# Optimization experiments

Hardware: AMD Instinct MI355X
Metric: run time of the kernel (lower is better)

## Reference

```python
import jax, jax.numpy as jnp
import numpy as np
from jax import lax

SCALES = [0.5, 0.25, 0.125, 0.0625]
D_MODEL = 256
IN_CH = 1


def setup_inputs() -> dict:
    key = jax.random.key(0)
    ks = jax.random.split(key, 16)
    x = jax.random.normal(ks[0], (2, D_MODEL, 256, 256), dtype=jnp.float32)
    m = jax.random.uniform(ks[1], (2, IN_CH, 256, 256), dtype=jnp.float32)
    s = 0.05
    Wq = jax.random.normal(ks[2], (D_MODEL, D_MODEL, 1, 1), jnp.float32) * s
    bq = jax.random.normal(ks[3], (D_MODEL,), jnp.float32) * s
    Wk = jax.random.normal(ks[4], (D_MODEL, D_MODEL, 1, 1), jnp.float32) * s
    bk = jax.random.normal(ks[5], (D_MODEL,), jnp.float32) * s
    Wv = jax.random.normal(ks[6], (D_MODEL, D_MODEL, 1, 1), jnp.float32) * s
    bv = jax.random.normal(ks[7], (D_MODEL,), jnp.float32) * s
    Wmq = jax.random.normal(ks[8], (D_MODEL, IN_CH, 1, 1), jnp.float32) * s
    bmq = jax.random.normal(ks[9], (D_MODEL,), jnp.float32) * s
    Wmk = jax.random.normal(ks[10], (D_MODEL, IN_CH, 1, 1), jnp.float32) * s
    bmk = jax.random.normal(ks[11], (D_MODEL,), jnp.float32) * s
    Wo = jax.random.normal(ks[12], (D_MODEL, D_MODEL, 3, 3), jnp.float32) * s
    bo = jax.random.normal(ks[13], (D_MODEL,), jnp.float32) * s
    return {"x": x, "m": m, "Wq": Wq, "bq": bq, "Wk": Wk, "bk": bk,
            "Wv": Wv, "bv": bv, "Wmq": Wmq, "bmq": bmq, "Wmk": Wmk, "bmk": bmk,
            "Wo": Wo, "bo": bo, "b": 1, "c": 256}


def _conv1x1(z, W, bias):
    # W: (O, I, 1, 1)
    return jnp.einsum('bihw,oi->bohw', z, W[:, :, 0, 0]) + bias[None, :, None, None]


def _forward(x, m, Wq, bq, Wk, bk, Wv, bv, Wmq, bmq, Wmk, bmk, Wo, bo, b, c):
    bt, _, h, w = x.shape  # h, w are multiples of 64 -> pad is zero
    t = bt // b
    n_scales = len(SCALES)
    d_k = c // n_scales

    q = _conv1x1(x, Wq, bq)
    k = _conv1x1(x, Wk, bk)
    v = _conv1x1(x, Wv, bv)
    mq = _conv1x1(m, Wmq, bmq)
    mk = _conv1x1(m, Wmk, bmk)

    outs = []
    for i, scale in enumerate(SCALES):
        height, width = int(h * scale), int(w * scale)
        out_h, out_w = h // height, w // width
        sl = slice(i * d_k, (i + 1) * d_k)

        def patch(z):
            # (b, t, d_k, out_h, height, out_w, width) -> (b, t*out_h*out_w, d_k*height*width)
            z = z[:, sl].reshape(b, t, d_k, out_h, height, out_w, width)
            z = z.transpose(0, 1, 3, 5, 2, 4, 6)
            return z.reshape(b, t * out_h * out_w, d_k * height * width)

        Q, K, V = patch(q), patch(k), patch(v)
        MQ, MK = patch(mq), patch(mk)
        inv_sqrt_d = 1.0 / jnp.sqrt(jnp.asarray(Q.shape[-1], jnp.float32))
        scores = jnp.einsum('bnd,bmd->bnm', Q, K) * inv_sqrt_d
        mask_scores = jnp.einsum('bnd,bmd->bnm', MQ, MK) * inv_sqrt_d
        p_attn = jax.nn.softmax(scores * mask_scores, axis=-1)
        y = jnp.einsum('bnm,bmd->bnd', p_attn, V)
        # back to (bt, d_k, h, w)
        y = y.reshape(b, t, out_h, out_w, d_k, height, width)
        y = y.transpose(0, 1, 4, 2, 5, 3, 6).reshape(bt, d_k, h, w)
        outs.append(y)

    out = jnp.concatenate(outs, axis=1)
    z = lax.conv_general_dilated(out, Wo, window_strides=(1, 1),
                                 padding=((1, 1), (1, 1)),
                                 dimension_numbers=('NCHW', 'OIHW', 'NCHW'))
    z = z + bo[None, :, None, None]
    return jnp.where(z > 0, z, 0.2 * z)  # LeakyReLU(0.2)


def reference(x, m, Wq, bq, Wk, bk, Wv, bv, Wmq, bmq, Wmk, bmk, Wo, bo, b, c):
    return _forward(x, m, Wq, bq, Wk, bk, Wv, bv, Wmq, bmq, Wmk, bmk, Wo, bo, b, c)
```

## Files before the change

kernel.cpp:

```cpp
#include <hip/hip_runtime.h>
#include <stdint.h>


typedef __attribute__((ext_vector_type(8))) short short8;
typedef __attribute__((ext_vector_type(4))) float floatx4;
typedef __attribute__((ext_vector_type(4))) unsigned int uintx4;

#define DEV static __device__ __forceinline__

DEV unsigned short f2bf(float f) {
  unsigned u = __builtin_bit_cast(unsigned, f);
  unsigned r = u + 0x7FFFu + ((u >> 16) & 1u);
  return (unsigned short)(r >> 16);
}

DEV void patch_row(int n, int sc, int lw, int& pt, int& sp0) {
  pt = n >> (2 + 2 * sc);
  int rem = n & ((4 << (2 * sc)) - 1);
  int oh = rem >> (1 + sc), ow = rem & ((2 << sc) - 1);
  sp0 = (oh << (lw + 8)) + (ow << lw);
}

__global__ void k_prep(const float* __restrict__ Wq, const float* __restrict__ Wk,
                       const float* __restrict__ Wv, const float* __restrict__ bq,
                       const float* __restrict__ bk, const float* __restrict__ bv,
                       const float* __restrict__ Wmq, const float* __restrict__ bmq,
                       const float* __restrict__ Wmk, const float* __restrict__ bmk,
                       const float* __restrict__ Wo, const float* __restrict__ bo,
                       unsigned short* __restrict__ wqkv, float* __restrict__ bias,
                       float* __restrict__ msc, unsigned short* __restrict__ wobf,
                       float* __restrict__ scoresG, unsigned int* __restrict__ pbuf) {
  int bid = blockIdx.x;
  int t = threadIdx.x;
  if (bid < 768) {
    const float* src = bid < 256 ? (Wq + bid * 256) : (bid < 512 ? (Wk + (bid - 256) * 256)
                                                                 : (Wv + (bid - 512) * 256));
    wqkv[bid * 256 + t] = f2bf(src[t]);
    if (t == 0) bias[bid] = bid < 256 ? bq[bid] : (bid < 512 ? bk[bid - 256] : bv[bid - 512]);
    return;
  }
  if (bid == 768) {
    int sc = t >> 6, lane = t & 63;
    int ch = sc * 64 + lane;
    float a0 = Wmq[ch] * Wmk[ch];
    float a1 = Wmq[ch] * bmk[ch];
    float a2 = bmq[ch] * Wmk[ch];
    float a3 = bmq[ch] * bmk[ch];
    for (int off = 32; off; off >>= 1) {
      a0 += __shfl_xor(a0, off); a1 += __shfl_xor(a1, off);
      a2 += __shfl_xor(a2, off); a3 += __shfl_xor(a3, off);
    }
    if (lane == 0) {
      msc[sc * 4 + 0] = a0; msc[sc * 4 + 1] = a1;
      msc[sc * 4 + 2] = a2; msc[sc * 4 + 3] = a3;
    }
    return;
  }
  int blk = bid - 769;
  if (blk < 2304) {
    int didx = blk >> 8, o = blk & 255, c = t;
    wobf[didx * 65536 + o * 256 + c] = f2bf(Wo[o * 2304 + c * 9 + didx]);
  } else {
    int i = (blk - 2304) * 256 + t;
    if (i < 559232) scoresG[i] = 0.f;
    if (i < 140032) pbuf[i] = 0u;
  }
}

__global__ __launch_bounds__(256) void k_xt(const float* __restrict__ x,
                                            unsigned short* __restrict__ xt) {
  __shared__ __align__(16) unsigned short tile[64][72];
  int p0 = blockIdx.x * 64, c0 = blockIdx.y * 64, t = blockIdx.z;
  int tid = threadIdx.x;
  {
    int cc = tid >> 2, pq = (tid & 3) * 16;
    const float* src = x + ((t * 256 + c0 + cc) * 65536 + p0 + pq);
    __align__(16) unsigned short tmp[16];
#pragma unroll
    for (int e = 0; e < 16; e += 4) {
      floatx4 v = *(const floatx4*)(src + e);
      tmp[e + 0] = f2bf(v[0]); tmp[e + 1] = f2bf(v[1]);
      tmp[e + 2] = f2bf(v[2]); tmp[e + 3] = f2bf(v[3]);
    }
    *(uintx4*)&tile[cc][pq] = *(const uintx4*)&tmp[0];
    *(uintx4*)&tile[cc][pq + 8] = *(const uintx4*)&tmp[8];
  }
  __syncthreads();
  {
    int pp = tid >> 2, cg = (tid & 3) * 16;
    __align__(16) unsigned short outv[16];
#pragma unroll
    for (int e = 0; e < 16; ++e) outv[e] = tile[cg + e][pp];
    unsigned short* dst = xt + ((t * 65536 + p0 + pp) * 256 + c0 + cg);
    *(uintx4*)dst = *(const uintx4*)&outv[0];
    *(uintx4*)(dst + 8) = *(const uintx4*)&outv[8];
  }
}

__global__ __launch_bounds__(256) void k_yt(const unsigned short* __restrict__ ynat,
                                            unsigned short* __restrict__ yt) {
  __shared__ __align__(16) unsigned short tile[64][72];
  int p0 = blockIdx.x * 64, c0 = blockIdx.y * 64, t = blockIdx.z;
  int tid = threadIdx.x;
  {
    int cc = tid >> 2, pq = (tid & 3) * 16;
    const unsigned short* src = ynat + ((t * 256 + c0 + cc) * 65536 + p0 + pq);
    *(uintx4*)&tile[cc][pq] = *(const uintx4*)src;
    *(uintx4*)&tile[cc][pq + 8] = *(const uintx4*)(src + 8);
  }
  __syncthreads();
  {
    int pp = tid >> 2, cg = (tid & 3) * 16;
    __align__(16) unsigned short outv[16];
#pragma unroll
    for (int e = 0; e < 16; ++e) outv[e] = tile[cg + e][pp];
    unsigned short* dst = yt + ((t * 65536 + p0 + pp) * 256 + c0 + cg);
    *(uintx4*)dst = *(const uintx4*)&outv[0];
    *(uintx4*)(dst + 8) = *(const uintx4*)&outv[8];
  }
}

__global__ __launch_bounds__(256, 2) void k_qkv(const unsigned short* __restrict__ xt,
                                                const unsigned short* __restrict__ wqkv,
                                                const float* __restrict__ bias,
                                                unsigned short* __restrict__ qkv) {
  extern __shared__ __align__(16) char smem[];
  auto As = (unsigned short (*)[64])(smem);
  auto Bs = (unsigned short (*)[64])(smem + 16384);
  auto Cs = (unsigned short (*)[280])(smem);
  int flat = blockIdx.x;
  int lg = (flat & 7) * 384 + (flat >> 3);
  int n_t = lg / 6, m_t = lg - n_t * 6;
  int n0 = n_t << 8, m0 = m_t << 7;
  int tid = threadIdx.x;
  int w = tid >> 6, l = tid & 63;
  int wr = w >> 1, wc = w & 1;
  int l15 = l & 15, lhi = l >> 4;
  int sr = tid >> 1, sbase = (tid & 1) * 4, r7 = sr & 7;
  int b7 = tid & 7;
  const unsigned short* gA = wqkv + (m0 + sr) * 256 + sbase * 8;
  const unsigned short* gB = xt + (n0 + tid) * 256;
  floatx4 zf = {0.f, 0.f, 0.f, 0.f};
  floatx4 acc[4][8];
#pragma unroll
  for (int i = 0; i < 4; ++i)
#pragma unroll
    for (int j = 0; j < 8; ++j) acc[i][j] = zf;
  uintx4 ra[4], rb[8];
#define QLOAD(K0) { const uintx4* pa = (const uintx4*)(gA + (K0)); \
                    ra[0] = pa[0]; ra[1] = pa[1]; ra[2] = pa[2]; ra[3] = pa[3]; \
                    const uintx4* pb = (const uintx4*)(gB + (K0)); \
                    rb[0] = pb[0]; rb[1] = pb[1]; rb[2] = pb[2]; rb[3] = pb[3]; \
                    rb[4] = pb[4]; rb[5] = pb[5]; rb[6] = pb[6]; rb[7] = pb[7]; }
  QLOAD(0);
#pragma unroll
  for (int ch = 0; ch < 4; ++ch) {
    __syncthreads();
#pragma unroll
    for (int j = 0; j < 4; ++j)
      *(uintx4*)&As[sr][((sbase + j) ^ r7) * 8] = ra[j];
#pragma unroll
    for (int j = 0; j < 8; ++j)
      *(uintx4*)&Bs[tid][(j ^ b7) * 8] = rb[j];
    __syncthreads();
    if (ch < 3) QLOAD((ch + 1) * 64);
#pragma unroll
    for (int kk = 0; kk < 2; ++kk) {
      short8 af[4];
#pragma unroll
      for (int f = 0; f < 4; ++f) {
        int arow = wr * 64 + f * 16 + l15;
        af[f] = *(const short8*)&As[arow][(((kk << 2) + lhi) ^ (arow & 7)) * 8];
      }
#pragma unroll
      for (int fn = 0; fn < 8; ++fn) {
        int brow = wc * 128 + fn * 16 + l15;
        short8 b = *(const short8*)&Bs[brow][(((kk << 2) + lhi) ^ (brow & 7)) * 8];
#pragma unroll
        for (int fm = 0; fm < 4; ++fm)
          acc[fm][fn] = __builtin_amdgcn_mfma_f32_16x16x32_bf16(af[fm], b, acc[fm][fn], 0, 0, 0);
      }
    }
  }
#undef QLOAD
#pragma unroll
  for (int h = 0; h < 2; ++h) {
    __syncthreads();
    if (wr == h) {
#pragma unroll
      for (int fm = 0; fm < 4; ++fm) {
#pragma unroll
        for (int rr = 0; rr < 4; ++rr) {
          int rl = fm * 16 + lhi * 4 + rr;
          float bv = bias[m0 + h * 64 + rl];
#pragma unroll
          for (int fn = 0; fn < 8; ++fn)
            Cs[rl][wc * 128 + fn * 16 + l15] = f2bf(acc[fm][fn][rr] + bv);
        }
      }
    }
    __syncthreads();
    {
      int p8 = (tid & 31) * 8;
      int pcol = n0 + p8;
      int t = pcol >> 16, p = pcol & 65535;
#pragma unroll
      for (int pass = 0; pass < 8; ++pass) {
        int rl = (tid >> 5) + pass * 8;
        uintx4 v = *(const uintx4*)&Cs[rl][p8];
        *(uintx4*)&qkv[((t * 768 + m0 + h * 64 + rl) << 16) + p] = v;
      }
    }
  }
}

__global__ __launch_bounds__(256) void k_mask(const float* __restrict__ m,
                                              float* __restrict__ G,
                                              float* __restrict__ rbuf) {
  int bid = blockIdx.x;
  int tid = threadIdx.x;
  if (bid >= 328) {
    int row = (bid - 328) * 4 + (tid >> 6);
    int lane = tid & 63;
    if (row < 680) {
      int sc, n;
      if (row < 8)        { sc = 0; n = row; }
      else if (row < 40)  { sc = 1; n = row - 8; }
      else if (row < 168) { sc = 2; n = row - 40; }
      else                { sc = 3; n = row - 168; }
      int lw = 7 - sc, W = 1 << lw;
      int pt, sp0;
      patch_row(n, sc, lw, pt, sp0);
      int base = pt * 65536 + sp0;
      int S = 1 << (14 - 2 * sc);
      float acc = 0.f;
      for (int s = lane; s < S; s += 64) {
        int hh = s >> lw, ww = s & (W - 1);
        acc += m[base + (hh << 8) + ww];
      }
      for (int off = 32; off; off >>= 1) acc += __shfl_xor(acc, off);
      if (lane == 0) rbuf[row] = acc;
    }
    return;
  }
  __shared__ __align__(16) float Ns[32][68];
// ... 9 lines not shown
  bool isA = tid < 128;
  int u = tid & 127;
  int srow = u >> 2, sslot0 = (u & 3) * 4;
  int grow = (isA ? n0 : m0) + srow;
  bool valid = grow < N;
  int pt = 0, sp0 = 0;
  if (valid) patch_row(grow, sc, lw, pt, sp0);
  int gbase = pt * 65536 + sp0;
  int trc = tid >> 4, tcc = tid & 15;
  float a00 = 0.f, a01 = 0.f, a10 = 0.f, a11 = 0.f;
  floatx4 zf = {0.f, 0.f, 0.f, 0.f};
  for (int c = 0; c < nchunks; ++c) {
    int k0 = kbase + c * 64;
    floatx4 v[4];
#pragma unroll
    for (int j = 0; j < 4; ++j) {
      v[j] = zf;
      if (valid) {
        int s = k0 + (sslot0 + j) * 4;
        int hh = s >> lw, ww = s & (W - 1);
        v[j] = *(const floatx4*)(m + gbase + (hh << 8) + ww);
      }
    }
    __syncthreads();
    float* dstrow = isA ? &Ns[srow][0] : &Ms[srow][0];
#pragma unroll
    for (int j = 0; j < 4; ++j) *(floatx4*)&dstrow[(sslot0 + j) * 4] = v[j];
    __syncthreads();
#pragma unroll 4
    for (int k = 0; k < 64; k += 4) {
      floatx4 na = *(const floatx4*)&Ns[2 * trc][k];
      floatx4 nb = *(const floatx4*)&Ns[2 * trc + 1][k];
      floatx4 ma = *(const floatx4*)&Ms[2 * tcc][k];
      floatx4 mb = *(const floatx4*)&Ms[2 * tcc + 1][k];
#pragma unroll
      for (int e = 0; e < 4; ++e) {
        a00 += na[e] * ma[e]; a01 += na[e] * mb[e];
        a10 += nb[e] * ma[e]; a11 += nb[e] * mb[e];
      }
    }
  }
  int rn = n0 + 2 * trc, rm = m0 + 2 * tcc;
  float res[2][2] = {{a00, a01}, {a10, a11}};
#pragma unroll
  for (int i = 0; i < 2; ++i)
#pragma unroll
    for (int j = 0; j < 2; ++j) {
      if (rn + i < N && rm + j < N) {
        float* dst = &G[soff + (rn + i) * N + rm + j];
        if (sc < 3) atomicAdd(dst, res[i][j]); else *dst = res[i][j];
      }
    }
}

__global__ __launch_bounds__(256) void k_scores_all(const unsigned short* __restrict__ qkv,
                                                    float* __restrict__ scores) {
  __shared__ __align__(16) char sbuf[32768];
  int bid = blockIdx.x;
  int tid = threadIdx.x;
  int w = tid >> 6, l = tid & 63;
  int wr = w >> 1, wc = w & 1, l15 = l & 15, lhi = l >> 4;
  uintx4 zu = {0u, 0u, 0u, 0u};
  floatx4 zf = {0.f, 0.f, 0.f, 0.f};
  if (bid < 160) {
    auto As = (unsigned short (*)[64])(sbuf);
    auto Bs = (unsigned short (*)[64])(sbuf + 16384);
    int lg = (bid & 7) * 20 + (bid >> 3);
    int sc, tn, tm, z, soff;
    if (lg < 32) { sc = 2; tn = 0; tm = 0; z = lg; soff = 1088; }
    else { int r = lg - 32; int tl = r >> 3; sc = 3; tn = tl >> 2; tm = tl & 3; z = r & 7; soff = 17472; }
    int N = 8 << (2 * sc);
    int lw = 7 - sc, W = 1 << lw, lS = 14 - 2 * sc;
    int n0 = tn * 128, m0 = tm * 128;
    int kbase = z * 2048;
    int sr = tid >> 1, sbase = (tid & 1) * 4, r7 = sr & 7;
    int ptA, spA, ptB, spB;
    patch_row(n0 + sr, sc, lw, ptA, spA);
    patch_row(m0 + sr, sc, lw, ptB, spB);
    int baseA = (ptA * 768 + sc * 64) * 65536 + spA;
    int baseB = (ptB * 768 + 256 + sc * 64) * 65536 + spB;
    floatx4 acc[4][4];
#pragma unroll
    for (int i = 0; i < 4; ++i)
#pragma unroll
      for (int j = 0; j < 4; ++j) acc[i][j] = zf;
    uintx4 ra[4], rb[4];
#define GLOAD(K0) { \
  _Pragma("unroll") for (int j = 0; j < 4; ++j) { \
    int k = kbase + (K0) + (sbase + j) * 8; \
    int cl = k >> lS; int s = k & ((1 << lS) - 1); \
    int hh = s >> lw, ww = s & (W - 1); \
    int off = cl * 65536 + (hh << 8) + ww; \
    ra[j] = *(const uintx4*)(qkv + baseA + off); \
    rb[j] = *(const uintx4*)(qkv + baseB + off); } }
    GLOAD(0);
    for (int st = 0; st < 32; ++st) {
      __syncthreads();
#pragma unroll
      for (int j = 0; j < 4; ++j) {
        *(uintx4*)&As[sr][((sbase + j) ^ r7) * 8] = ra[j];
        *(uintx4*)&Bs[sr][((sbase + j) ^ r7) * 8] = rb[j];
      }
      __syncthreads();
      if (st < 31) GLOAD((st + 1) * 64);
#pragma unroll
      for (int kk = 0; kk < 2; ++kk) {
        short8 af[4], bfr[4];
#pragma unroll
        for (int f = 0; f < 4; ++f) {
          int arow = wr * 64 + f * 16 + l15;
          af[f] = *(const short8*)&As[arow][(((kk << 2) + lhi) ^ (arow & 7)) * 8];
          int brow = wc * 64 + f * 16 + l15;
          bfr[f] = *(const short8*)&Bs[brow][(((kk << 2) + lhi) ^ (brow & 7)) * 8];
        }
#pragma unroll
        for (int fm = 0; fm < 4; ++fm)
#pragma unroll
          for (int fn = 0; fn < 4; ++fn)
            acc[fm][fn] = __builtin_amdgcn_mfma_f32_16x16x32_bf16(af[fm], bfr[fn], acc[fm][fn], 0, 0, 0);
      }
    }
#undef GLOAD
#pragma unroll
    for (int fm = 0; fm < 4; ++fm) {
      int nrow = n0 + wr * 64 + fm * 16 + lhi * 4;
#pragma unroll
      for (int rr = 0; rr < 4; ++rr) {
#pragma unroll
        for (int fn = 0; fn < 4; ++fn) {
          int mcol = m0 + wc * 64 + fn * 16 + l15;
          atomicAdd(&scores[soff + (nrow + rr) * N + mcol], acc[fm][fn][rr]);
        }
      }
    }
    return;
  }
  {
    auto As = (unsigned short (*)[136])(sbuf);
    auto Bs = (unsigned short (*)[136])(sbuf + 8704);
    int b2 = bid - 160;
    int sc, z, soff;
    if (b2 < 256) { sc = 0; z = b2;       soff = 0; }
    else          { sc = 1; z = b2 - 256; soff = 64; }
    int lw = 7 - sc, W = 1 << lw, lS = 14 - 2 * sc, N = 8 << (2 * sc);
    int kbase = z * 4096;
    floatx4 acc = zf;
    bool isA = tid < 128;
    int u = tid & 127;
    int srow = u >> 2, sslot0 = (u & 3) * 4;
    int grow = srow;
    int cb = (isA ? 0 : 256) + sc * 64;
    int pt = 0, sp0 = 0;
    bool valid = grow < N;
    if (valid) patch_row(grow, sc, lw, pt, sp0);
    int rowbase = (pt * 768 + cb) * 65536 + sp0;
    uintx4 r[4];
#define SLOAD(KS) { int kb2 = kbase + (KS) * 128; \
  _Pragma("unroll") for (int j = 0; j < 4; ++j) { \
    uintx4 v = zu; \
    if (valid) { int k = kb2 + (sslot0 + j) * 8; \
      int cl = k >> lS; int s = k & ((1 << lS) - 1); \
      int hh = s >> lw, ww = s & (W - 1); \
      v = *(const uintx4*)(qkv + rowbase + cl * 65536 + (hh << 8) + ww); } \
    r[j] = v; } }
    SLOAD(0);
    for (int ks = 0; ks < 32; ++ks) {
      __syncthreads();
      {
        unsigned short* dstrow = isA ? &As[srow][0] : &Bs[srow][0];
#pragma unroll
        for (int j = 0; j < 4; ++j) *(uintx4*)&dstrow[(sslot0 + j) * 8] = r[j];
      }
      __syncthreads();
// ... 39 lines not shown
    float v = -1e30f;
    int mcol = lane + j * 64;
    if (j * 64 < N && mcol < N) {
      float sq = scores[soff + n * N + mcol];
      float g = G[soff + n * N + mcol];
      float rm = rbuf[roff + mcol];
      v = sq * (alpha * g + beta * rn + gamma * rm + delta * Sf) * invD;
    }
    vals[j] = v;
    mx = fmaxf(mx, v);
  }
  for (int off = 32; off; off >>= 1) mx = fmaxf(mx, __shfl_xor(mx, off));
  float sum = 0.f;
#pragma unroll
  for (int j = 0; j < 8; ++j) {
    int mcol = lane + j * 64;
    float e = 0.f;
    if (j * 64 < N && mcol < N) e = __expf(vals[j] - mx);
    vals[j] = e;
    sum += e;
  }
  for (int off = 32; off; off >>= 1) sum += __shfl_xor(sum, off);
  float inv = 1.f / sum;
#pragma unroll
  for (int j = 0; j < 8; ++j) {
    int mcol = lane + j * 64;
    if (j * 64 < N && mcol < N) pbuf[poff + n * Kpad + mcol] = f2bf(vals[j] * inv);
  }
}

__global__ __launch_bounds__(256) void k_pv(const unsigned short* __restrict__ qkv,
                                            const unsigned short* __restrict__ pbuf,
                                            unsigned short* __restrict__ ynat) {
  int bid = blockIdx.x;
  int sc, bx, by;
  if (bid < 4096)      { sc = 0; bx = bid; by = 0; }
  else if (bid < 6144) { sc = 1; bx = bid - 4096; by = 0; }
  else if (bid < 8192) { int r = bid - 6144; sc = 2; bx = r >> 1; by = r & 1; }
  else                 { int r = bid - 8192; sc = 3; bx = r >> 3; by = r & 7; }
  int WR    = (sc == 0) ? 1 : (sc == 1) ? 2 : 4;
  int logWC = (sc == 0) ? 2 : (sc == 1) ? 1 : 0;
  int poff  = (sc == 0) ? 0 : (sc == 1) ? 512 : (sc == 2) ? 1536 : 17920;
  int lw = 7 - sc, W = 1 << lw;
  int lS = 14 - 2 * sc;
  int N = 8 << (2 * sc);
  int Kpad = (sc < 2) ? 32 : N;
  int WC = 1 << logWC;
  int d0 = bx * (WC * 64);
  int nb = by * (WR * 16);
  __shared__ __align__(16) unsigned short As[2][64][40];
  __shared__ __align__(16) unsigned short Bt[2][256][32];
  int tid = threadIdx.x;
  int w = tid >> 6, l = tid & 63;
  int wr = w >> logWC, wc = w & (WC - 1);
  int l15 = l & 15, lhi = l >> 4;
  floatx4 zf = {0.f, 0.f, 0.f, 0.f};
  floatx4 acc[4];
#pragma unroll
  for (int i = 0; i < 4; ++i) acc[i] = zf;
  int bmp = tid & 15;
  int dg = tid >> 4;
  bool act0 = (WC > 1) || (dg < 8);
  bool has1 = (WC == 4);
  bool doA = tid < WR * 64;
  int arow = tid >> 2, akg = (tid & 3) * 8;
  int ksteps = Kpad >> 5;
  uintx4 zu = {0u, 0u, 0u, 0u};
// ... 45 lines not shown
    }
    __syncthreads();
    if (ks + 1 < ksteps) PLOADS(ks + 1);
    short8 a = *(const short8*)&As[b][wr * 16 + l15][lhi * 8];
#pragma unroll
    for (int fn = 0; fn < 4; ++fn) {
      int row = wc * 64 + fn * 16 + l15;
      int slot = lhi ^ ((row >> 1) & 3) ^ ((row >> 3) & 3);
      short8 bb = *(const short8*)&Bt[b][row][slot * 8];
      acc[fn] = __builtin_amdgcn_mfma_f32_16x16x32_bf16(a, bb, acc[fn], 0, 0, 0);
    }
  }
#undef PLOADS
  int nrow = nb + wr * 16 + lhi * 4;
#pragma unroll
  for (int rr = 0; rr < 4; ++rr) {
    int n = nrow + rr;
    if (n < N) {
      int pt, sp0;
      patch_row(n, sc, lw, pt, sp0);
#pragma unroll
      for (int fn = 0; fn < 4; ++fn) {
        int d = d0 + wc * 64 + fn * 16 + l15;
        int cl = d >> lS;
        int s = d & ((1 << lS) - 1);
        int hh = s >> lw, ww = s & (W - 1);
        int c = sc * 64 + cl;
        ynat[(pt * 256 + c) * 65536 + sp0 + (hh << 8) + ww] = f2bf(acc[fn][rr]);
      }
    }
  }
}

__global__ __launch_bounds__(256, 3) void k_conv(const unsigned short* __restrict__ yt,
                                                 const unsigned short* __restrict__ wo,
                                                 const float* __restrict__ bo,
                                                 float* __restrict__ out) {
  __shared__ __align__(16) unsigned short As[64][128];
  __shared__ __align__(16) unsigned short Bs[130][64];
  int flat = blockIdx.x;
  int lg = ((flat & 7) << 8) + (flat >> 3);
  int n_t = lg >> 2, m_t = lg & 3;
  int n0 = n_t << 8, m0 = m_t << 6;
  int tt = n0 >> 16, yy = (n0 >> 8) & 255;
  int tid = threadIdx.x;
  int w = tid >> 6, l = tid & 63;
  int l15 = l & 15, lhi = l >> 4;
  bool doA = tid < 192;
  int a_dx = tid >> 6, a_o = tid & 63;
  bool doBh = tid >= 254;
  floatx4 zf = {0.f, 0.f, 0.f, 0.f};
  floatx4 acc[4][4];
#pragma unroll
  for (int i = 0; i < 4; ++i)
#pragma unroll
    for (int j = 0; j < 4; ++j) acc[i][j] = zf;
  uintx4 zu = {0u, 0u, 0u, 0u};
  uintx4 rb[4], ra[4], rh[4];
  const unsigned short* ybase = yt + (tt << 24);
#define CLOAD(ST) { \
    int dy = (ST) >> 3, cc = ((ST) & 7) << 5; \
    int yq = yy + dy - 1; \
    bool yv = (unsigned)yq < 256u; \
    { int xq = tid - 1; \
      if (yv && (unsigned)xq < 256u) { \
        const uintx4* p = (const uintx4*)(ybase + ((yq << 8) + xq) * 256 + cc); \
        rb[0] = p[0]; rb[1] = p[1]; rb[2] = p[2]; rb[3] = p[3]; \
      } else { rb[0] = zu; rb[1] = zu; rb[2] = zu; rb[3] = zu; } } \
    if (doA) { \
      const uintx4* p = (const uintx4*)(wo + (dy * 3 + a_dx) * 65536 + (m0 + a_o) * 256 + cc); \
      ra[0] = p[0]; ra[1] = p[1]; ra[2] = p[2]; ra[3] = p[3]; \
    } else if (doBh) { \
      int xq = tid + 1;   \
      if (yv && xq < 256) { \
        const uintx4* p = (const uintx4*)(ybase + ((yq << 8) + xq) * 256 + cc); \
        rh[0] = p[0]; rh[1] = p[1]; rh[2] = p[2]; rh[3] = p[3]; \
      } else { rh[0] = zu; rh[1] = zu; rh[2] = zu; rh[3] = zu; } } }
  CLOAD(0);
  for (int st = 0; st < 24; ++st) {
    __syncthreads();
    {
      int brow = tid >> 1, bhf = (tid & 1) * 4, br7 = brow & 7;
#pragma unroll
      for (int j = 0; j < 4; ++j)
        *(uintx4*)&Bs[brow][((bhf + j) ^ br7) * 8] = rb[j];
      if (doA) {
        int o7 = a_o & 7;
#pragma unroll
        for (int j = 0; j < 4; ++j)
          *(uintx4*)&As[a_o][((a_dx * 4 + j) ^ o7) * 8] = ra[j];
      } else if (doBh) {
        int xh = tid + 2;
        int brow2 = xh >> 1, bhf2 = (xh & 1) * 4, br72 = brow2 & 7;
#pragma unroll
        for (int j = 0; j < 4; ++j)
          *(uintx4*)&Bs[brow2][((bhf2 + j) ^ br72) * 8] = rh[j];
      }
    }
    __syncthreads();
    if (st < 23) CLOAD(st + 1);
#pragma unroll
    for (int dx = 0; dx < 3; ++dx) {
      short8 af[4];
#pragma unroll
      for (int f = 0; f < 4; ++f) {
        int ol = f * 16 + l15;
        af[f] = *(const short8*)&As[ol][((dx * 4 + lhi) ^ (ol & 7)) * 8];
      }
#pragma unroll
      for (int fn = 0; fn < 4; ++fn) {
        int xh = w * 64 + fn * 16 + l15 + dx;
        short8 b = *(const short8*)&Bs[xh >> 1][((((xh & 1) * 4 + lhi)) ^ ((xh >> 1) & 7)) * 8];
#pragma unroll
        for (int fm = 0; fm < 4; ++fm)
          acc[fm][fn] = __builtin_amdgcn_mfma_f32_16x16x32_bf16(af[fm], b, acc[fm][fn], 0, 0, 0);
      }
    }
  }
#undef CLOAD
#pragma unroll
  for (int fm = 0; fm < 4; ++fm) {
    int o = m0 + fm * 16 + lhi * 4;
#pragma unroll
    for (int rr = 0; rr < 4; ++rr) {
      float bias = bo[o + rr];
#pragma unroll
      for (int fn = 0; fn < 4; ++fn) {
        int xcol = w * 64 + fn * 16 + l15;
        float z = acc[fm][fn][rr] + bias;
        out[((tt * 256 + o + rr) << 16) + (yy << 8) + xcol] = z > 0.f ? z : 0.2f * z;
      }
    }
  }
}

extern "C" void kernel_launch(void* const* d_in, const int* in_sizes, int n_in,
                              void* d_out, int out_size, void* d_ws, size_t ws_size,
                              hipStream_t stream) {
  const float* x   = (const float*)d_in[0];
  const float* m   = (const float*)d_in[1];
  const float* Wq  = (const float*)d_in[2];
  const float* bq  = (const float*)d_in[3];
  const float* Wk  = (const float*)d_in[4];
  const float* bk  = (const float*)d_in[5];
  const float* Wv  = (const float*)d_in[6];
  const float* bv  = (const float*)d_in[7];
  const float* Wmq = (const float*)d_in[8];
  const float* bmq = (const float*)d_in[9];
  const float* Wmk = (const float*)d_in[10];
  const float* bmk = (const float*)d_in[11];
  const float* Wo  = (const float*)d_in[12];
  const float* bo  = (const float*)d_in[13];

  char* ws = (char*)d_ws;
  unsigned short* qkv   = (unsigned short*)(ws);
  unsigned short* xtb   = (unsigned short*)(ws + 201326592);
  unsigned short* wqkv  = (unsigned short*)(ws + 268435456);
  unsigned short* wobf  = (unsigned short*)(ws + 268828672);
  float* bias           = (float*)(ws + 270008320);
  float* msc            = (float*)(ws + 270011392);
  float* scores         = (float*)(ws + 270011456);
  float* G              = (float*)(ws + 271129920);
  float* rbuf           = (float*)(ws + 272248384);
  unsigned short* pbuf  = (unsigned short*)(ws + 272251104);
  float* out            = (float*)d_out;
  unsigned short* ynat  = (unsigned short*)d_out;

  k_prep<<<dim3(5258), dim3(256), 0, stream>>>(Wq, Wk, Wv, bq, bk, bv, Wmq, bmq, Wmk, bmk,
                                               Wo, bo, wqkv, bias, msc, wobf, scores,
                                               (unsigned int*)pbuf);
  k_xt<<<dim3(1024, 4, 2), dim3(256), 0, stream>>>(x, xtb);
  k_qkv<<<dim3(3072), dim3(256), 49152, stream>>>(xtb, wqkv, bias, qkv);
  k_mask<<<dim3(498), dim3(256), 0, stream>>>(m, G, rbuf);
  k_scores_all<<<dim3(480), dim3(256), 0, stream>>>(qkv, scores);
  k_softmax<<<dim3(680), dim3(64), 0, stream>>>(scores, G, rbuf, msc, pbuf);
  k_pv<<<dim3(10240), dim3(256), 0, stream>>>(qkv, pbuf, ynat);
  k_yt<<<dim3(1024, 4, 2), dim3(256), 0, stream>>>(ynat, xtb);
  k_conv<<<dim3(2048), dim3(256), 0, stream>>>(xtb, wobf, bo, out);
}
```

Before: 576.4 us.

## Retile 3x3 conv as full-row GEMM, split scores K more, remap PV blocks

The output 3x3 conv is rebuilt as a 512-thread block computing all 256 output channels for a full image row. It uses a tap-major weight layout (o, tap, c) and a double-buffered LDS pipeline over 36 K-steps, replacing the previous 64-channel tiles with halo handling. The split-K factor for the small-scale score GEMMs is doubled to give more blocks, at the cost of more atomic adds. PV block indices for the larger scales are permuted for better cache locality, and some kernels are reordered in the file. The larger conv tile raises register and LDS use and cuts occupancy to one block per CU, with fewer blocks overall.

```diff
diff --git a/kernel.cpp b/kernel.cpp
--- a/kernel.cpp
+++ b/kernel.cpp
@@ -21,14 +21,14 @@
   sp0 = (oh << (lw + 8)) + (ow << lw);
 }
 
-__global__ void k_prep(const float* __restrict__ Wq, const float* __restrict__ Wk,
+__global__ __launch_bounds__(256) void k_prep(const float* __restrict__ Wq, const float* __restrict__ Wk,
                        const float* __restrict__ Wv, const float* __restrict__ bq,
                        const float* __restrict__ bk, const float* __restrict__ bv,
                        const float* __restrict__ Wmq, const float* __restrict__ bmq,
                        const float* __restrict__ Wmk, const float* __restrict__ bmk,
-                       const float* __restrict__ Wo, const float* __restrict__ bo,
+                       const float* __restrict__ Wo,
                        unsigned short* __restrict__ wqkv, float* __restrict__ bias,
-                       float* __restrict__ msc, unsigned short* __restrict__ wobf,
+                       float* __restrict__ msc, unsigned short* __restrict__ wo3,
                        float* __restrict__ scoresG, unsigned int* __restrict__ pbuf) {
   int bid = blockIdx.x;
   int t = threadIdx.x;
@@ -59,158 +59,11 @@
   int blk = bid - 769;
   if (blk < 2304) {
     int didx = blk >> 8, o = blk & 255, c = t;
-    wobf[didx * 65536 + o * 256 + c] = f2bf(Wo[o * 2304 + c * 9 + didx]);
+    wo3[o * 2304 + didx * 256 + c] = f2bf(Wo[o * 2304 + c * 9 + didx]);
   } else {
     int i = (blk - 2304) * 256 + t;
     if (i < 559232) scoresG[i] = 0.f;
     if (i < 140032) pbuf[i] = 0u;
-  }
-}
-
-__global__ __launch_bounds__(256) void k_xt(const float* __restrict__ x,
-                                            unsigned short* __restrict__ xt) {
-  __shared__ __align__(16) unsigned short tile[64][72];
-  int p0 = blockIdx.x * 64, c0 = blockIdx.y * 64, t = blockIdx.z;
-  int tid = threadIdx.x;
-  {
-    int cc = tid >> 2, pq = (tid & 3) * 16;
-    const float* src = x + ((t * 256 + c0 + cc) * 65536 + p0 + pq);
-    __align__(16) unsigned short tmp[16];
-#pragma unroll
-    for (int e = 0; e < 16; e += 4) {
-      floatx4 v = *(const floatx4*)(src + e);
-      tmp[e + 0] = f2bf(v[0]); tmp[e + 1] = f2bf(v[1]);
-      tmp[e + 2] = f2bf(v[2]); tmp[e + 3] = f2bf(v[3]);
-    }
-    *(uintx4*)&tile[cc][pq] = *(const uintx4*)&tmp[0];
-    *(uintx4*)&tile[cc][pq + 8] = *(const uintx4*)&tmp[8];
-  }
-  __syncthreads();
-  {
-    int pp = tid >> 2, cg = (tid & 3) * 16;
-    __align__(16) unsigned short outv[16];
-#pragma unroll
-    for (int e = 0; e < 16; ++e) outv[e] = tile[cg + e][pp];
-    unsigned short* dst = xt + ((t * 65536 + p0 + pp) * 256 + c0 + cg);
-    *(uintx4*)dst = *(const uintx4*)&outv[0];
-    *(uintx4*)(dst + 8) = *(const uintx4*)&outv[8];
-  }
-}
-
-__global__ __launch_bounds__(256) void k_yt(const unsigned short* __restrict__ ynat,
-                                            unsigned short* __restrict__ yt) {
-  __shared__ __align__(16) unsigned short tile[64][72];
-  int p0 = blockIdx.x * 64, c0 = blockIdx.y * 64, t = blockIdx.z;
-  int tid = threadIdx.x;
-  {
-    int cc = tid >> 2, pq = (tid & 3) * 16;
-    const unsigned short* src = ynat + ((t * 256 + c0 + cc) * 65536 + p0 + pq);
-    *(uintx4*)&tile[cc][pq] = *(const uintx4*)src;
-    *(uintx4*)&tile[cc][pq + 8] = *(const uintx4*)(src + 8);
-  }
-  __syncthreads();
-  {
-    int pp = tid >> 2, cg = (tid & 3) * 16;
-    __align__(16) unsigned short outv[16];
-#pragma unroll
-    for (int e = 0; e < 16; ++e) outv[e] = tile[cg + e][pp];
-    unsigned short* dst = yt + ((t * 65536 + p0 + pp) * 256 + c0 + cg);
-    *(uintx4*)dst = *(const uintx4*)&outv[0];
-    *(uintx4*)(dst + 8) = *(const uintx4*)&outv[8];
-  }
-}
-
-__global__ __launch_bounds__(256, 2) void k_qkv(const unsigned short* __restrict__ xt,
-                                                const unsigned short* __restrict__ wqkv,
-                                                const float* __restrict__ bias,
-                                                unsigned short* __restrict__ qkv) {
-  extern __shared__ __align__(16) char smem[];
-  auto As = (unsigned short (*)[64])(smem);
-  auto Bs = (unsigned short (*)[64])(smem + 16384);
-  auto Cs = (unsigned short (*)[280])(smem);
-  int flat = blockIdx.x;
-  int lg = (flat & 7) * 384 + (flat >> 3);
-  int n_t = lg / 6, m_t = lg - n_t * 6;
-  int n0 = n_t << 8, m0 = m_t << 7;
-  int tid = threadIdx.x;
-  int w = tid >> 6, l = tid & 63;
-  int wr = w >> 1, wc = w & 1;
-  int l15 = l & 15, lhi = l >> 4;
-  int sr = tid >> 1, sbase = (tid & 1) * 4, r7 = sr & 7;
-  int b7 = tid & 7;
-  const unsigned short* gA = wqkv + (m0 + sr) * 256 + sbase * 8;
-  const unsigned short* gB = xt + (n0 + tid) * 256;
-  floatx4 zf = {0.f, 0.f, 0.f, 0.f};
-  floatx4 acc[4][8];
-#pragma unroll
-  for (int i = 0; i < 4; ++i)
-#pragma unroll
-    for (int j = 0; j < 8; ++j) acc[i][j] = zf;
-  uintx4 ra[4], rb[8];
-#define QLOAD(K0) { const uintx4* pa = (const uintx4*)(gA + (K0)); \
-                    ra[0] = pa[0]; ra[1] = pa[1]; ra[2] = pa[2]; ra[3] = pa[3]; \
-                    const uintx4* pb = (const uintx4*)(gB + (K0)); \
-                    rb[0] = pb[0]; rb[1] = pb[1]; rb[2] = pb[2]; rb[3] = pb[3]; \
-                    rb[4] = pb[4]; rb[5] = pb[5]; rb[6] = pb[6]; rb[7] = pb[7]; }
-  QLOAD(0);
-#pragma unroll
-  for (int ch = 0; ch < 4; ++ch) {
-    __syncthreads();
-#pragma unroll
-    for (int j = 0; j < 4; ++j)
-      *(uintx4*)&As[sr][((sbase + j) ^ r7) * 8] = ra[j];
-#pragma unroll
-    for (int j = 0; j < 8; ++j)
-      *(uintx4*)&Bs[tid][(j ^ b7) * 8] = rb[j];
-    __syncthreads();
-    if (ch < 3) QLOAD((ch + 1) * 64);
-#pragma unroll
-    for (int kk = 0; kk < 2; ++kk) {
-      short8 af[4];
-#pragma unroll
-      for (int f = 0; f < 4; ++f) {
-        int arow = wr * 64 + f * 16 + l15;
-        af[f] = *(const short8*)&As[arow][(((kk << 2) + lhi) ^ (arow & 7)) * 8];
-      }
-#pragma unroll
-      for (int fn = 0; fn < 8; ++fn) {
-        int brow = wc * 128 + fn * 16 + l15;
-        short8 b = *(const short8*)&Bs[brow][(((kk << 2) + lhi) ^ (brow & 7)) * 8];
-#pragma unroll
-        for (int fm = 0; fm < 4; ++fm)
-          acc[fm][fn] = __builtin_amdgcn_mfma_f32_16x16x32_bf16(af[fm], b, acc[fm][fn], 0, 0, 0);
-      }
-    }
-  }
-#undef QLOAD
-#pragma unroll
-  for (int h = 0; h < 2; ++h) {
-    __syncthreads();
-    if (wr == h) {
-#pragma unroll
-      for (int fm = 0; fm < 4; ++fm) {
-#pragma unroll
-        for (int rr = 0; rr < 4; ++rr) {
-          int rl = fm * 16 + lhi * 4 + rr;
-          float bv = bias[m0 + h * 64 + rl];
-#pragma unroll
-          for (int fn = 0; fn < 8; ++fn)
-            Cs[rl][wc * 128 + fn * 16 + l15] = f2bf(acc[fm][fn][rr] + bv);
-        }
-      }
-    }
-    __syncthreads();
-    {
-      int p8 = (tid & 31) * 8;
-      int pcol = n0 + p8;
-      int t = pcol >> 16, p = pcol & 65535;
-#pragma unroll
-      for (int pass = 0; pass < 8; ++pass) {
-        int rl = (tid >> 5) + pass * 8;
-        uintx4 v = *(const uintx4*)&Cs[rl][p8];
-        *(uintx4*)&qkv[((t * 768 + m0 + h * 64 + rl) << 16) + p] = v;
-      }
-    }
   }
 }
 
@@ -286,11 +139,11 @@
       floatx4 na = *(const floatx4*)&Ns[2 * trc][k];
       floatx4 nb = *(const floatx4*)&Ns[2 * trc + 1][k];
       floatx4 ma = *(const floatx4*)&Ms[2 * tcc][k];
-      floatx4 mb = *(const floatx4*)&Ms[2 * tcc + 1][k];
+      floatx4 mb2 = *(const floatx4*)&Ms[2 * tcc + 1][k];
 #pragma unroll
       for (int e = 0; e < 4; ++e) {
-        a00 += na[e] * ma[e]; a01 += na[e] * mb[e];
-        a10 += nb[e] * ma[e]; a11 += nb[e] * mb[e];
+        a00 += na[e] * ma[e]; a01 += na[e] * mb2[e];
+        a10 += nb[e] * ma[e]; a11 += nb[e] * mb2[e];
       }
     }
   }
@@ -305,6 +158,153 @@
         if (sc < 3) atomicAdd(dst, res[i][j]); else *dst = res[i][j];
       }
     }
+}
+
+__global__ __launch_bounds__(256) void k_xt(const float* __restrict__ x,
+                                            unsigned short* __restrict__ xt) {
+  __shared__ __align__(16) unsigned short tile[64][72];
+  int p0 = blockIdx.x * 64, c0 = blockIdx.y * 64, t = blockIdx.z;
+  int tid = threadIdx.x;
+  {
+    int cc = tid >> 2, pq = (tid & 3) * 16;
+    const float* src = x + ((t * 256 + c0 + cc) * 65536 + p0 + pq);
+    __align__(16) unsigned short tmp[16];
+#pragma unroll
+    for (int e = 0; e < 16; e += 4) {
+      floatx4 v = *(const floatx4*)(src + e);
+      tmp[e + 0] = f2bf(v[0]); tmp[e + 1] = f2bf(v[1]);
+      tmp[e + 2] = f2bf(v[2]); tmp[e + 3] = f2bf(v[3]);
+    }
+    *(uintx4*)&tile[cc][pq] = *(const uintx4*)&tmp[0];
+    *(uintx4*)&tile[cc][pq + 8] = *(const uintx4*)&tmp[8];
+  }
+  __syncthreads();
+  {
+    int pp = tid >> 2, cg = (tid & 3) * 16;
+    __align__(16) unsigned short outv[16];
+#pragma unroll
+    for (int e = 0; e < 16; ++e) outv[e] = tile[cg + e][pp];
+    unsigned short* dst = xt + ((t * 65536 + p0 + pp) * 256 + c0 + cg);
+    *(uintx4*)dst = *(const uintx4*)&outv[0];
+    *(uintx4*)(dst + 8) = *(const uintx4*)&outv[8];
+  }
+}
+
+__global__ __launch_bounds__(256) void k_yt(const unsigned short* __restrict__ ynat,
+                                            unsigned short* __restrict__ yt) {
+  __shared__ __align__(16) unsigned short tile[64][72];
+  int p0 = blockIdx.x * 64, c0 = blockIdx.y * 64, t = blockIdx.z;
+  int tid = threadIdx.x;
+  {
+    int cc = tid >> 2, pq = (tid & 3) * 16;
+    const unsigned short* src = ynat + ((t * 256 + c0 + cc) * 65536 + p0 + pq);
+    *(uintx4*)&tile[cc][pq] = *(const uintx4*)src;
+    *(uintx4*)&tile[cc][pq + 8] = *(const uintx4*)(src + 8);
+  }
+  __syncthreads();
+  {
+    int pp = tid >> 2, cg = (tid & 3) * 16;
+    __align__(16) unsigned short outv[16];
+#pragma unroll
+    for (int e = 0; e < 16; ++e) outv[e] = tile[cg + e][pp];
+    unsigned short* dst = yt + ((t * 65536 + p0 + pp) * 256 + c0 + cg);
+    *(uintx4*)dst = *(const uintx4*)&outv[0];
+    *(uintx4*)(dst + 8) = *(const uintx4*)&outv[8];
+  }
+}
+
+__global__ __launch_bounds__(256, 2) void k_qkv(const unsigned short* __restrict__ xt,
+                                                const unsigned short* __restrict__ wqkv,
+                                                const float* __restrict__ bias,
+                                                unsigned short* __restrict__ qkv) {
+  extern __shared__ __align__(16) char smem[];
+  auto As = (unsigned short (*)[64])(smem);
+  auto Bs = (unsigned short (*)[64])(smem + 16384);
+  auto Cs = (unsigned short (*)[280])(smem);
+  int flat = blockIdx.x;
+  int lg = (flat & 7) * 384 + (flat >> 3);
+  int n_t = lg / 6, m_t = lg - n_t * 6;
+  int n0 = n_t << 8, m0 = m_t << 7;
+  int tid = threadIdx.x;
+  int w = tid >> 6, l = tid & 63;
+  int wr = w >> 1, wc = w & 1;
+  int l15 = l & 15, lhi = l >> 4;
+  int sr = tid >> 1, sbase = (tid & 1) * 4, r7 = sr & 7;
+  int b7 = tid & 7;
+  const unsigned short* gA = wqkv + (m0 + sr) * 256 + sbase * 8;
+  const unsigned short* gB = xt + (n0 + tid) * 256;
+  floatx4 zf = {0.f, 0.f, 0.f, 0.f};
+  floatx4 acc[4][8];
+#pragma unroll
+  for (int i = 0; i < 4; ++i)
+#pragma unroll
+    for (int j = 0; j < 8; ++j) acc[i][j] = zf;
+  uintx4 ra[4], rb[8];
+#define QLOAD(K0) { const uintx4* pa = (const uintx4*)(gA + (K0)); \
+                    ra[0] = pa[0]; ra[1] = pa[1]; ra[2] = pa[2]; ra[3] = pa[3]; \
+                    const uintx4* pb = (const uintx4*)(gB + (K0)); \
+                    rb[0] = pb[0]; rb[1] = pb[1]; rb[2] = pb[2]; rb[3] = pb[3]; \
+                    rb[4] = pb[4]; rb[5] = pb[5]; rb[6] = pb[6]; rb[7] = pb[7]; }
+  QLOAD(0);
+#pragma unroll
+  for (int ch = 0; ch < 4; ++ch) {
+    __syncthreads();
+#pragma unroll
+    for (int j = 0; j < 4; ++j)
+      *(uintx4*)&As[sr][((sbase + j) ^ r7) * 8] = ra[j];
+#pragma unroll
+    for (int j = 0; j < 8; ++j)
+      *(uintx4*)&Bs[tid][(j ^ b7) * 8] = rb[j];
+    __syncthreads();
+    if (ch < 3) QLOAD((ch + 1) * 64);
+#pragma unroll
+    for (int kk = 0; kk < 2; ++kk) {
+      short8 af[4];
+#pragma unroll
+      for (int f = 0; f < 4; ++f) {
+        int arow = wr * 64 + f * 16 + l15;
+        af[f] = *(const short8*)&As[arow][(((kk << 2) + lhi) ^ (arow & 7)) * 8];
+      }
+#pragma unroll
+      for (int fn = 0; fn < 8; ++fn) {
+        int brow = wc * 128 + fn * 16 + l15;
+        short8 b = *(const short8*)&Bs[brow][(((kk << 2) + lhi) ^ (brow & 7)) * 8];
+#pragma unroll
+        for (int fm = 0; fm < 4; ++fm)
+          acc[fm][fn] = __builtin_amdgcn_mfma_f32_16x16x32_bf16(af[fm], b, acc[fm][fn], 0, 0, 0);
+      }
+    }
+  }
+#undef QLOAD
+#pragma unroll
+  for (int h = 0; h < 2; ++h) {
+    __syncthreads();
+    if (wr == h) {
+#pragma unroll
+      for (int fm = 0; fm < 4; ++fm) {
+#pragma unroll
+        for (int rr = 0; rr < 4; ++rr) {
+          int rl = fm * 16 + lhi * 4 + rr;
+          float bv = bias[m0 + h * 64 + rl];
+#pragma unroll
+          for (int fn = 0; fn < 8; ++fn)
+            Cs[rl][wc * 128 + fn * 16 + l15] = f2bf(acc[fm][fn][rr] + bv);
+        }
+      }
+    }
+    __syncthreads();
+    {
+      int p8 = (tid & 31) * 8;
+      int pcol = n0 + p8;
+      int t = pcol >> 16, p = pcol & 65535;
+#pragma unroll
+      for (int pass = 0; pass < 8; ++pass) {
+        int rl = (tid >> 5) + pass * 8;
+        uintx4 v = *(const uintx4*)&Cs[rl][p8];
+        *(uintx4*)&qkv[((t * 768 + m0 + h * 64 + rl) << 16) + p] = v;
+      }
+    }
+  }
 }
 
 __global__ __launch_bounds__(256) void k_scores_all(const unsigned short* __restrict__ qkv,
@@ -316,17 +316,17 @@
   int wr = w >> 1, wc = w & 1, l15 = l & 15, lhi = l >> 4;
   uintx4 zu = {0u, 0u, 0u, 0u};
   floatx4 zf = {0.f, 0.f, 0.f, 0.f};
-  if (bid < 160) {
+  if (bid < 320) {
     auto As = (unsigned short (*)[64])(sbuf);
     auto Bs = (unsigned short (*)[64])(sbuf + 16384);
-    int lg = (bid & 7) * 20 + (bid >> 3);
+    int lg = (bid & 7) * 40 + (bid >> 3);
     int sc, tn, tm, z, soff;
-    if (lg < 32) { sc = 2; tn = 0; tm = 0; z = lg; soff = 1088; }
-    else { int r = lg - 32; int tl = r >> 3; sc = 3; tn = tl >> 2; tm = tl & 3; z = r & 7; soff = 17472; }
+    if (lg < 64) { sc = 2; tn = 0; tm = 0; z = lg; soff = 1088; }
+    else { int r = lg - 64; int tl = r >> 4; sc = 3; tn = tl >> 2; tm = tl & 3; z = r & 15; soff = 17472; }
     int N = 8 << (2 * sc);
     int lw = 7 - sc, W = 1 << lw, lS = 14 - 2 * sc;
     int n0 = tn * 128, m0 = tm * 128;
-    int kbase = z * 2048;
+    int kbase = z * 1024;
     int sr = tid >> 1, sbase = (tid & 1) * 4, r7 = sr & 7;
     int ptA, spA, ptB, spB;
     patch_row(n0 + sr, sc, lw, ptA, spA);
@@ -348,7 +348,7 @@
     ra[j] = *(const uintx4*)(qkv + baseA + off); \
     rb[j] = *(const uintx4*)(qkv + baseB + off); } }
     GLOAD(0);
-    for (int st = 0; st < 32; ++st) {
+    for (int st = 0; st < 16; ++st) {
       __syncthreads();
 #pragma unroll
       for (int j = 0; j < 4; ++j) {
@@ -356,7 +356,7 @@
         *(uintx4*)&Bs[sr][((sbase + j) ^ r7) * 8] = rb[j];
       }
       __syncthreads();
-      if (st < 31) GLOAD((st + 1) * 64);
+      if (st < 15) GLOAD((st + 1) * 64);
 #pragma unroll
       for (int kk = 0; kk < 2; ++kk) {
         short8 af[4], bfr[4];
@@ -392,7 +392,7 @@
   {
     auto As = (unsigned short (*)[136])(sbuf);
     auto Bs = (unsigned short (*)[136])(sbuf + 8704);
-    int b2 = bid - 160;
+    int b2 = bid - 320;
     int sc, z, soff;
     if (b2 < 256) { sc = 0; z = b2;       soff = 0; }
     else          { sc = 1; z = b2 - 256; soff = 64; }
@@ -498,7 +498,17 @@
 __global__ __launch_bounds__(256) void k_pv(const unsigned short* __restrict__ qkv,
                                             const unsigned short* __restrict__ pbuf,
                                             unsigned short* __restrict__ ynat) {
-  int bid = blockIdx.x;
+  int bid0 = blockIdx.x;
+  int bid;
+  if (bid0 < 6144) {
+    bid = bid0;
+  } else if (bid0 < 8192) {
+    int q = bid0 - 6144; int c = q & 7, j = q >> 3;
+    bid = 6144 + ((c * 128 + (j & 127)) << 1) + (j >> 7);
+  } else {
+    int q = bid0 - 8192; int c = q & 7, j = q >> 3;
+    bid = 8192 + ((c * 32 + (j & 31)) << 3) + (j >> 5);
+  }
   int sc, bx, by;
   if (bid < 4096)      { sc = 0; bx = bid; by = 0; }
   else if (bid < 6144) { sc = 1; bx = bid - 4096; by = 0; }
@@ -610,101 +620,79 @@
   }
 }
 
-__global__ __launch_bounds__(256, 3) void k_conv(const unsigned short* __restrict__ yt,
-                                                 const unsigned short* __restrict__ wo,
+__global__ __launch_bounds__(512, 1) void k_conv(const unsigned short* __restrict__ yt,
+                                                 const unsigned short* __restrict__ wo3,
                                                  const float* __restrict__ bo,
                                                  float* __restrict__ out) {
-  __shared__ __align__(16) unsigned short As[64][128];
-  __shared__ __align__(16) unsigned short Bs[130][64];
+  __shared__ __align__(16) unsigned short Asm[2][256][64];
+  __shared__ __align__(16) unsigned short Bsm[2][256][64];
   int flat = blockIdx.x;
-  int lg = ((flat & 7) << 8) + (flat >> 3);
-  int n_t = lg >> 2, m_t = lg & 3;
-  int n0 = n_t << 8, m0 = m_t << 6;
-  int tt = n0 >> 16, yy = (n0 >> 8) & 255;
+  int lg = (flat & 7) * 64 + (flat >> 3);
+  int tt = lg >> 8, yy = lg & 255;
   int tid = threadIdx.x;
   int w = tid >> 6, l = tid & 63;
+  int wr = w >> 2, wc = w & 3;
   int l15 = l & 15, lhi = l >> 4;
-  bool doA = tid < 192;
-  int a_dx = tid >> 6, a_o = tid & 63;
-  bool doBh = tid >= 254;
+  int sr = tid >> 1, sbase = (tid & 1) * 4, r7 = sr & 7;
+  const unsigned short* gA = wo3 + sr * 2304 + sbase * 8;
+  const unsigned short* ybase = yt + (tt << 24);
   floatx4 zf = {0.f, 0.f, 0.f, 0.f};
-  floatx4 acc[4][4];
-#pragma unroll
-  for (int i = 0; i < 4; ++i)
+  floatx4 acc[8][4];
+#pragma unroll
+  for (int i = 0; i < 8; ++i)
 #pragma unroll
     for (int j = 0; j < 4; ++j) acc[i][j] = zf;
   uintx4 zu = {0u, 0u, 0u, 0u};
-  uintx4 rb[4], ra[4], rh[4];
-  const unsigned short* ybase = yt + (tt << 24);
+  uintx4 ra[4], rb[4];
 #define CLOAD(ST) { \
-    int dy = (ST) >> 3, cc = ((ST) & 7) << 5; \
-    int yq = yy + dy - 1; \
-    bool yv = (unsigned)yq < 256u; \
-    { int xq = tid - 1; \
-      if (yv && (unsigned)xq < 256u) { \
-        const uintx4* p = (const uintx4*)(ybase + ((yq << 8) + xq) * 256 + cc); \
-        rb[0] = p[0]; rb[1] = p[1]; rb[2] = p[2]; rb[3] = p[3]; \
-      } else { rb[0] = zu; rb[1] = zu; rb[2] = zu; rb[3] = zu; } } \
-    if (doA) { \
-      const uintx4* p = (const uintx4*)(wo + (dy * 3 + a_dx) * 65536 + (m0 + a_o) * 256 + cc); \
-      ra[0] = p[0]; ra[1] = p[1]; ra[2] = p[2]; ra[3] = p[3]; \
-    } else if (doBh) { \
-      int xq = tid + 1;   \
-      if (yv && xq < 256) { \
-        const uintx4* p = (const uintx4*)(ybase + ((yq << 8) + xq) * 256 + cc); \
-        rh[0] = p[0]; rh[1] = p[1]; rh[2] = p[2]; rh[3] = p[3]; \
-      } else { rh[0] = zu; rh[1] = zu; rh[2] = zu; rh[3] = zu; } } }
+    const uintx4* pa = (const uintx4*)(gA + (ST) * 64); \
+    ra[0] = pa[0]; ra[1] = pa[1]; ra[2] = pa[2]; ra[3] = pa[3]; \
+    int tap = (ST) >> 2, ch0 = ((ST) & 3) << 6; \
+    int dy3 = (tap * 11) >> 5; int dy = dy3 - 1; int dx = tap - dy3 * 3 - 1; \
+    int yq = yy + dy, xq = sr + dx; \
+    if (((unsigned)yq < 256u) && ((unsigned)xq < 256u)) { \
+      const uintx4* pb = (const uintx4*)(ybase + ((yq << 8) + xq) * 256 + ch0 + sbase * 8); \
+      rb[0] = pb[0]; rb[1] = pb[1]; rb[2] = pb[2]; rb[3] = pb[3]; \
+    } else { rb[0] = zu; rb[1] = zu; rb[2] = zu; rb[3] = zu; } }
   CLOAD(0);
-  for (int st = 0; st < 24; ++st) {
-    __syncthreads();
-    {
-      int brow = tid >> 1, bhf = (tid & 1) * 4, br7 = brow & 7;
-#pragma unroll
-      for (int j = 0; j < 4; ++j)
-        *(uintx4*)&Bs[brow][((bhf + j) ^ br7) * 8] = rb[j];
-      if (doA) {
-        int o7 = a_o & 7;
-#pragma unroll
-        for (int j = 0; j < 4; ++j)
-          *(uintx4*)&As[a_o][((a_dx * 4 + j) ^ o7) * 8] = ra[j];
-      } else if (doBh) {
-        int xh = tid + 2;
-        int brow2 = xh >> 1, bhf2 = (xh & 1) * 4, br72 = brow2 & 7;
-#pragma unroll
-        for (int j = 0; j < 4; ++j)
-          *(uintx4*)&Bs[brow2][((bhf2 + j) ^ br72) * 8] = rh[j];
-      }
-    }
-    __syncthreads();
-    if (st < 23) CLOAD(st + 1);
-#pragma unroll
-    for (int dx = 0; dx < 3; ++dx) {
-      short8 af[4];
-#pragma unroll
-      for (int f = 0; f < 4; ++f) {
-        int ol = f * 16 + l15;
-        af[f] = *(const short8*)&As[ol][((dx * 4 + lhi) ^ (ol & 7)) * 8];
-      }
+  for (int st = 0; st < 36; ++st) {
+    int cur = st & 1;
+    __syncthreads();
+#pragma unroll
+    for (int j = 0; j < 4; ++j) {
+      *(uintx4*)&Asm[cur][sr][((sbase + j) ^ r7) * 8] = ra[j];
+      *(uintx4*)&Bsm[cur][sr][((sbase + j) ^ r7) * 8] = rb[j];
+    }
+    __syncthreads();
+    if (st < 35) CLOAD(st + 1);
+#pragma unroll
+    for (int kk = 0; kk < 2; ++kk) {
+      short8 bf[4];
 #pragma unroll
       for (int fn = 0; fn < 4; ++fn) {
-        int xh = w * 64 + fn * 16 + l15 + dx;
-        short8 b = *(const short8*)&Bs[xh >> 1][((((xh & 1) * 4 + lhi)) ^ ((xh >> 1) & 7)) * 8];
-#pragma unroll
-        for (int fm = 0; fm < 4; ++fm)
-          acc[fm][fn] = __builtin_amdgcn_mfma_f32_16x16x32_bf16(af[fm], b, acc[fm][fn], 0, 0, 0);
+        int brow = wc * 64 + fn * 16 + l15;
+        bf[fn] = *(const short8*)&Bsm[cur][brow][(((kk << 2) + lhi) ^ (brow & 7)) * 8];
+      }
+#pragma unroll
+      for (int fm = 0; fm < 8; ++fm) {
+        int arow = wr * 128 + fm * 16 + l15;
+        short8 af = *(const short8*)&Asm[cur][arow][(((kk << 2) + lhi) ^ (arow & 7)) * 8];
+#pragma unroll
+        for (int fn = 0; fn < 4; ++fn)
+          acc[fm][fn] = __builtin_amdgcn_mfma_f32_16x16x32_bf16(af, bf[fn], acc[fm][fn], 0, 0, 0);
       }
     }
   }
 #undef CLOAD
 #pragma unroll
-  for (int fm = 0; fm < 4; ++fm) {
-    int o = m0 + fm * 16 + lhi * 4;
+  for (int fm = 0; fm < 8; ++fm) {
+    int o = wr * 128 + fm * 16 + lhi * 4;
 #pragma unroll
     for (int rr = 0; rr < 4; ++rr) {
       float bias = bo[o + rr];
 #pragma unroll
       for (int fn = 0; fn < 4; ++fn) {
-        int xcol = w * 64 + fn * 16 + l15;
+        int xcol = wc * 64 + fn * 16 + l15;
         float z = acc[fm][fn][rr] + bias;
         out[((tt * 256 + o + rr) << 16) + (yy << 8) + xcol] = z > 0.f ? z : 0.2f * z;
       }
@@ -734,7 +722,7 @@
   unsigned short* qkv   = (unsigned short*)(ws);
   unsigned short* xtb   = (unsigned short*)(ws + 201326592);
   unsigned short* wqkv  = (unsigned short*)(ws + 268435456);
-  unsigned short* wobf  = (unsigned short*)(ws + 268828672);
+  unsigned short* wo3   = (unsigned short*)(ws + 268828672);
   float* bias           = (float*)(ws + 270008320);
   float* msc            = (float*)(ws + 270011392);
   float* scores         = (float*)(ws + 270011456);
@@ -745,14 +733,14 @@
   unsigned short* ynat  = (unsigned short*)d_out;
 
   k_prep<<<dim3(5258), dim3(256), 0, stream>>>(Wq, Wk, Wv, bq, bk, bv, Wmq, bmq, Wmk, bmk,
-                                               Wo, bo, wqkv, bias, msc, wobf, scores,
+                                               Wo, wqkv, bias, msc, wo3, scores,
                                                (unsigned int*)pbuf);
   k_xt<<<dim3(1024, 4, 2), dim3(256), 0, stream>>>(x, xtb);
   k_qkv<<<dim3(3072), dim3(256), 49152, stream>>>(xtb, wqkv, bias, qkv);
   k_mask<<<dim3(498), dim3(256), 0, stream>>>(m, G, rbuf);
-  k_scores_all<<<dim3(480), dim3(256), 0, stream>>>(qkv, scores);
+  k_scores_all<<<dim3(640), dim3(256), 0, stream>>>(qkv, scores);
   k_softmax<<<dim3(680), dim3(64), 0, stream>>>(scores, G, rbuf, msc, pbuf);
   k_pv<<<dim3(10240), dim3(256), 0, stream>>>(qkv, pbuf, ynat);
   k_yt<<<dim3(1024, 4, 2), dim3(256), 0, stream>>>(ynat, xtb);
-  k_conv<<<dim3(2048), dim3(256), 0, stream>>>(xtb, wobf, bo, out);
-}
+  k_conv<<<dim3(512), dim3(512), 0, stream>>>(xtb, wo3, bo, out);
+}
```

Result: no change. 579.2 us (+0.5%).
